# Kernel optimization log

Measured on AMD Instinct MI355X. Metric: run time of the kernel, lower is better.

The kernel has to match this reference:

```python
import jax, jax.numpy as jnp
import numpy as np

DIM = 384
WS = 7
NH = 12
N = WS ** 3          # 343 tokens per window
BW = 256             # number of windows (batch*num_windows)
HD = DIM // NH       # head dim = 32


def _rel_pos_index(ws: int) -> np.ndarray:
    coords = np.stack(np.meshgrid(np.arange(ws), np.arange(ws), np.arange(ws), indexing='ij'))
    coords = coords.reshape(3, -1)                       # [3, N]
    rel = coords[:, :, None] - coords[:, None, :]        # [3, N, N]
    rel = rel.transpose(1, 2, 0)                         # [N, N, 3]
    rel = rel + (ws - 1)
    idx = rel[..., 0] * (2 * ws - 1) ** 2 + rel[..., 1] * (2 * ws - 1) + rel[..., 2]
    return idx.astype(np.int32)                          # [N, N]


def setup_inputs() -> dict:
    key = jax.random.key(0)
    ks = jax.random.split(key, 6)
    x = jax.random.normal(ks[0], (BW, N, DIM), dtype=jnp.float32)
    qkv_w = jax.random.normal(ks[1], (DIM, 3 * DIM), dtype=jnp.float32) * (DIM ** -0.5)
    qkv_b = jax.random.normal(ks[2], (3 * DIM,), dtype=jnp.float32) * 0.02
    proj_w = jax.random.normal(ks[3], (DIM, DIM), dtype=jnp.float32) * (DIM ** -0.5)
    proj_b = jax.random.normal(ks[4], (DIM,), dtype=jnp.float32) * 0.02
    bias_table = jax.random.normal(ks[5], ((2 * WS - 1) ** 3, NH), dtype=jnp.float32) * 0.02
    rel_pos_index = jnp.asarray(_rel_pos_index(WS))
    return {"x": x, "qkv_w": qkv_w, "qkv_b": qkv_b, "proj_w": proj_w,
            "proj_b": proj_b, "bias_table": bias_table, "rel_pos_index": rel_pos_index}


def reference(x, qkv_w, qkv_b, proj_w, proj_b, bias_table, rel_pos_index):
    B_, n, C = x.shape
    scale = (C // NH) ** -0.5
    qkv = (x @ qkv_w + qkv_b).reshape(B_, n, 3, NH, C // NH)
    q, k, v = qkv[:, :, 0], qkv[:, :, 1], qkv[:, :, 2]   # [B_, n, H, d]
    # scores: [B_, H, n, n]
    attn = jnp.einsum('bihd,bjhd->bhij', q, k) * scale
    rel_bias = bias_table[rel_pos_index]                  # [n, n, H]
    attn = attn + rel_bias.transpose(2, 0, 1)[None]
    attn = jax.nn.softmax(attn, axis=-1)
    out = jnp.einsum('bhij,bjhd->bihd', attn, v).reshape(B_, n, C)
    return out @ proj_w + proj_b
```

## Files before the change

kernel.cpp:

```cpp
#include <hip/hip_runtime.h>


#define M_TOT 87808
#define NTOK  343
#define NPAD  352
#define DIMC  384
#define NHEAD 12
#define QKVN  1152
#define BWIN  256
#define BSLAB (NTOK * NPAD)

typedef __bf16 bf16x8 __attribute__((ext_vector_type(8)));
typedef __bf16 bf16x4 __attribute__((ext_vector_type(4)));
typedef float f32x4 __attribute__((ext_vector_type(4)));

__device__ __forceinline__ unsigned short bf16rne(float f) {
  unsigned int u = __float_as_uint(f);
  u += 0x7fffu + ((u >> 16) & 1u);
  return (unsigned short)(u >> 16);
}

__device__ __forceinline__ unsigned int packbf(float lo, float hi) {
  return (unsigned int)bf16rne(lo) | ((unsigned int)bf16rne(hi) << 16);
}

__device__ __forceinline__ bf16x4 pack_bf16x4(float a, float b, float c, float d) {
  unsigned ua = __float_as_uint(a) + 0x8000u;
  unsigned ub = __float_as_uint(b) + 0x8000u;
  unsigned uc = __float_as_uint(c) + 0x8000u;
  unsigned ud = __float_as_uint(d) + 0x8000u;
  unsigned lo = __builtin_amdgcn_perm(ub, ua, 0x07060302u);
  unsigned hi = __builtin_amdgcn_perm(ud, uc, 0x07060302u);
  union { unsigned u[2]; bf16x4 v; } x;
  x.u[0] = lo; x.u[1] = hi;
  return x.v;
}


__global__ void cvt_x_kernel(const float* __restrict__ x, unsigned short* __restrict__ xb, int n8) {
  int i = blockIdx.x * 256 + threadIdx.x;
  if (i >= n8) return;
  const float4* xv = (const float4*)x + (size_t)i * 2;
  float4 a = xv[0], b = xv[1];
  uint4 o;
  o.x = packbf(a.x, a.y); o.y = packbf(a.z, a.w);
  o.z = packbf(b.x, b.y); o.w = packbf(b.z, b.w);
  ((uint4*)xb)[i] = o;
}

__global__ void prep_w_kernel(const float* __restrict__ qkv_w, const float* __restrict__ proj_w,
                              unsigned short* __restrict__ wqkvT, unsigned short* __restrict__ wprojT) {
  int tid = blockIdx.x * 256 + threadIdx.x;
  if (tid < QKVN * DIMC) {
    int n = tid / DIMC, k = tid - n * DIMC;
    wqkvT[tid] = bf16rne(qkv_w[(size_t)k * QKVN + n]);
  }
  if (tid < DIMC * DIMC) {
    int n = tid / DIMC, k = tid - n * DIMC;
    wprojT[tid] = bf16rne(proj_w[(size_t)k * DIMC + n]);
  }
}

__global__ void prep_bias_kernel(const float* __restrict__ bias_table, const int* __restrict__ rel_idx,
                                 float* __restrict__ biasmat) {
  int tid = blockIdx.x * 256 + threadIdx.x;
  if (tid >= NTOK * NPAD) return;
  int i = tid / NPAD, j = tid - i * NPAD;
  const float LOG2E = 1.44269504088896340f;
  if (j < NTOK) {
    int idx = rel_idx[i * NTOK + j];
    #pragma unroll
    for (int h = 0; h < NHEAD; h++)
      biasmat[(size_t)h * BSLAB + tid] = bias_table[idx * NHEAD + h] * LOG2E;
  } else {
    #pragma unroll
    for (int h = 0; h < NHEAD; h++)
      biasmat[(size_t)h * BSLAB + tid] = -1e30f;
  }
}


typedef const __attribute__((address_space(1))) unsigned int* gas_t;
typedef __attribute__((address_space(3))) unsigned int* las_t;

__device__ __forceinline__ void load16_lds(const void* g, void* l) {
  __builtin_amdgcn_global_load_lds((gas_t)g, (las_t)l, 16, 0, 0);
}

template<int OUT_MODE>
__global__ __launch_bounds__(256, 3) void gemm_bt_kernel(
    const unsigned short* __restrict__ A, const unsigned short* __restrict__ Bt,
    const float* __restrict__ bias, void* __restrict__ outp,
    int M, int Nn, int K)
{
  __shared__ __attribute__((aligned(16))) unsigned short Atile[128 * 64];
  __shared__ __attribute__((aligned(16))) unsigned short Btile[128 * 64];
  const int t = threadIdx.x;
  const int lane = t & 63, w = t >> 6;
  const int q = lane >> 4, l15 = lane & 15;
  const int m0 = blockIdx.y * 128, n0 = blockIdx.x * 128;
  const int wm = w >> 1, wn = w & 1;

  f32x4 acc[4][4] = {};

  for (int kk = 0; kk < K; kk += 64) {
    #pragma unroll
    for (int i = 0; i < 4; i++) {
      int chunk = i * 256 + t;
      int r = chunk >> 3, cl = chunk & 7;
      int cg = cl ^ (r & 7);
      load16_lds(A + (size_t)(m0 + r) * K + kk + cg * 8, Atile + chunk * 8);
      load16_lds(Bt + (size_t)(n0 + r) * K + kk + cg * 8, Btile + chunk * 8);
    }
    __syncthreads();
    const bf16x8* As = (const bf16x8*)Atile;
    const bf16x8* Bs = (const bf16x8*)Btile;
    #pragma unroll
    for (int kq = 0; kq < 2; kq++) {
      bf16x8 af[4], bfr[4];
      #pragma unroll
      for (int mt = 0; mt < 4; mt++) {
        int m = wm * 64 + mt * 16 + l15;
        af[mt] = As[m * 8 + ((kq * 4 + q) ^ (m & 7))];
      }
      #pragma unroll
      for (int nt = 0; nt < 4; nt++) {
        int nr = wn * 64 + nt * 16 + l15;
        bfr[nt] = Bs[nr * 8 + ((kq * 4 + q) ^ (nr & 7))];
      }
      #pragma unroll
      for (int mt = 0; mt < 4; mt++)
        #pragma unroll
        for (int nt = 0; nt < 4; nt++)
          acc[mt][nt] = __builtin_amdgcn_mfma_f32_16x16x32_bf16(af[mt], bfr[nt], acc[mt][nt], 0, 0, 0);
    }
    __syncthreads();
  }

  #pragma unroll
  for (int nt = 0; nt < 4; nt++) {
    int nn = n0 + wn * 64 + nt * 16;
    float bv = bias[nn + l15];
    #pragma unroll
    for (int mt = 0; mt < 4; mt++) {
      int mb = m0 + wm * 64 + mt * 16 + q * 4;
      #pragma unroll
      for (int r = 0; r < 4; r++) {
        float v = acc[mt][nt][r] + bv;
        if (OUT_MODE == 0) {
          ((float*)outp)[(size_t)(mb + r) * Nn + nn + l15] = v;
        } else {
          int which = nn / DIMC;
          int hh = (nn - which * DIMC) >> 5;
          int d0 = nn & 16;
          size_t off = ((size_t)(which * NHEAD + hh) * M_TOT + (mb + r)) * 32 + d0 + l15;
          ((unsigned short*)outp)[off] = bf16rne(v);
        }
      }
    }
  }
}


#define VST 360

__global__ __launch_bounds__(512, 6) void attn_kernel(
    const unsigned short* __restrict__ qhead,
    const float* __restrict__ biasmat,
    unsigned short* __restrict__ attnout)
{
  __shared__ __attribute__((aligned(16))) unsigned short Klds[22 * 512];
  __shared__ __attribute__((aligned(16))) unsigned short Vt[32 * VST];
  const int bx = blockIdx.x;
  const int h = bx >> 8, b = bx & 255;
  const int t = threadIdx.x;
  const int lane = t & 63, w = t >> 6;
  const int q = lane >> 4, l15 = lane & 15;

  const unsigned short* Qslab = qhead + ((size_t)(0 * NHEAD + h) * M_TOT + (size_t)b * NTOK) * 32;
  const unsigned short* Kslab = qhead + ((size_t)(1 * NHEAD + h) * M_TOT + (size_t)b * NTOK) * 32;
  const unsigned short* Vslab = qhead + ((size_t)(2 * NHEAD + h) * M_TOT + (size_t)b * NTOK) * 32;

  for (int jt = w; jt < 22; jt += 8)
    load16_lds(Kslab + (size_t)(jt * 16 + l15) * 32 + q * 8, Klds + jt * 512 + lane * 8);

  for (int j = t; j < NTOK; j += 512) {
    #pragma unroll
    for (int c = 0; c < 4; c++) {
      uint4 vd = *(const uint4*)(Vslab + (size_t)j * 32 + c * 8);
      const unsigned short* vs = (const unsigned short*)&vd;
      #pragma unroll
      for (int u = 0; u < 8; u++)
        Vt[(c * 8 + u) * VST + j] = vs[u];
    }
  }
  for (int idx = t; idx < 32 * 16; idx += 512)
    Vt[(idx >> 4) * VST + NTOK + (idx & 15)] = 0;
  __syncthreads();

  const float* bh_bias = biasmat + (size_t)h * BSLAB;
  const float CS = 0.17677669529663689f * 1.44269504088896340f;

  for (int pr = w; pr < 11; pr += 8) {
    int i0 = pr * 32;
    int iqA = i0 + l15;      iqA = iqA > (NTOK - 1) ? (NTOK - 1) : iqA;
    int iqB = i0 + 16 + l15; iqB = iqB > (NTOK - 1) ? (NTOK - 1) : iqB;
    bf16x8 bqA = *(const bf16x8*)(Qslab + (size_t)iqA * 32 + q * 8);
    bf16x8 bqB = *(const bf16x8*)(Qslab + (size_t)iqB * 32 + q * 8);
    const float* browA = bh_bias + (size_t)iqA * NPAD + 4 * q;
    const float* browB = bh_bias + (size_t)iqB * NPAD + 4 * q;

    f32x4 oA0 = {0.f,0.f,0.f,0.f}, oA1 = {0.f,0.f,0.f,0.f};
    f32x4 oB0 = {0.f,0.f,0.f,0.f}, oB1 = {0.f,0.f,0.f,0.f};
    float denA = 0.f, denB = 0.f;

    #pragma unroll 2
    for (int jt = 0; jt < 22; jt++) {
      bf16x8 ak = *(const bf16x8*)(Klds + jt * 512 + lane * 8);
      f32x4 z = {0.f,0.f,0.f,0.f};
      f32x4 sA = __builtin_amdgcn_mfma_f32_16x16x32_bf16(ak, bqA, z, 0, 0, 0);
      f32x4 sB = __builtin_amdgcn_mfma_f32_16x16x32_bf16(ak, bqB, z, 0, 0, 0);
      f32x4 bA = *(const f32x4*)(browA + jt * 16);
      f32x4 bB = *(const f32x4*)(browB + jt * 16);
      float pA0 = __builtin_amdgcn_exp2f(fmaf(sA[0], CS, bA[0]));
      float pA1 = __builtin_amdgcn_exp2f(fmaf(sA[1], CS, bA[1]));
      float pA2 = __builtin_amdgcn_exp2f(fmaf(sA[2], CS, bA[2]));
      float pA3 = __builtin_amdgcn_exp2f(fmaf(sA[3], CS, bA[3]));
      float pB0 = __builtin_amdgcn_exp2f(fmaf(sB[0], CS, bB[0]));
      float pB1 = __builtin_amdgcn_exp2f(fmaf(sB[1], CS, bB[1]));
      float pB2 = __builtin_amdgcn_exp2f(fmaf(sB[2], CS, bB[2]));
      float pB3 = __builtin_amdgcn_exp2f(fmaf(sB[3], CS, bB[3]));
      denA += (pA0 + pA1) + (pA2 + pA3);
      denB += (pB0 + pB1) + (pB2 + pB3);
      bf16x4 pfA = pack_bf16x4(pA0, pA1, pA2, pA3);
      bf16x4 pfB = pack_bf16x4(pB0, pB1, pB2, pB3);
      bf16x4 vf0 = *(const bf16x4*)(Vt + l15 * VST + jt * 16 + 4 * q);
      bf16x4 vf1 = *(const bf16x4*)(Vt + (16 + l15) * VST + jt * 16 + 4 * q);
      oA0 = __builtin_amdgcn_mfma_f32_16x16x16bf16_1k(pfA, vf0, oA0, 0, 0, 0);
      oA1 = __builtin_amdgcn_mfma_f32_16x16x16bf16_1k(pfA, vf1, oA1, 0, 0, 0);
      oB0 = __builtin_amdgcn_mfma_f32_16x16x16bf16_1k(pfB, vf0, oB0, 0, 0, 0);
      oB1 = __builtin_amdgcn_mfma_f32_16x16x16bf16_1k(pfB, vf1, oB1, 0, 0, 0);
    }

    denA += __shfl_xor(denA, 16); denA += __shfl_xor(denA, 32);
    denB += __shfl_xor(denB, 16); denB += __shfl_xor(denB, 32);

    #pragma unroll
    for (int r = 0; r < 4; r++) {
      int rr = 4 * q + r;
      float dA = __shfl(denA, rr);
      float dB = __shfl(denB, rr);
      int iA = i0 + rr, iB = i0 + 16 + rr;
      if (iA < NTOK) {
        float inv = __builtin_amdgcn_rcpf(dA);
        size_t orow = ((size_t)b * NTOK + iA) * DIMC + h * 32;
        attnout[orow + l15]      = bf16rne(oA0[r] * inv);
        attnout[orow + 16 + l15] = bf16rne(oA1[r] * inv);
      }
      if (iB < NTOK) {
        float inv = __builtin_amdgcn_rcpf(dB);
        size_t orow = ((size_t)b * NTOK + iB) * DIMC + h * 32;
        attnout[orow + l15]      = bf16rne(oB0[r] * inv);
        attnout[orow + 16 + l15] = bf16rne(oB1[r] * inv);
      }
    }
  }
}


extern "C" void kernel_launch(void* const* d_in, const int* in_sizes, int n_in,
                              void* d_out, int out_size, void* d_ws, size_t ws_size,
                              hipStream_t stream) {
  const float* x          = (const float*)d_in[0];
  const float* qkv_w      = (const float*)d_in[1];
  const float* qkv_b      = (const float*)d_in[2];
  const float* proj_w     = (const float*)d_in[3];
  const float* proj_b     = (const float*)d_in[4];
  const float* bias_table = (const float*)d_in[5];
  const int*   rel_idx    = (const int*)d_in[6];

  char* p = (char*)d_ws;
  unsigned short* xb      = (unsigned short*)p; p += (size_t)M_TOT * DIMC * 2;
  unsigned short* wqkvT   = (unsigned short*)p; p += (size_t)QKVN * DIMC * 2;
  unsigned short* wprojT  = (unsigned short*)p; p += (size_t)DIMC * DIMC * 2;
  float*          biasmat = (float*)p;          p += (size_t)NHEAD * BSLAB * 4;
  unsigned short* qhead   = (unsigned short*)p; p += (size_t)3 * NHEAD * M_TOT * 32 * 2;
  unsigned short* attnout = (unsigned short*)p; p += (size_t)M_TOT * DIMC * 2;

  cvt_x_kernel<<<(M_TOT * DIMC / 8 + 255) / 256, 256, 0, stream>>>(x, xb, M_TOT * DIMC / 8);
  prep_w_kernel<<<(QKVN * DIMC + 255) / 256, 256, 0, stream>>>(qkv_w, proj_w, wqkvT, wprojT);
  prep_bias_kernel<<<(NTOK * NPAD + 255) / 256, 256, 0, stream>>>(bias_table, rel_idx, biasmat);
  gemm_bt_kernel<1><<<dim3(QKVN / 128, M_TOT / 128), 256, 0, stream>>>(
      xb, wqkvT, qkv_b, (void*)qhead, M_TOT, QKVN, DIMC);
  attn_kernel<<<BWIN * NHEAD, 512, 0, stream>>>(qhead, biasmat, attnout);
  gemm_bt_kernel<0><<<dim3(DIMC / 128, M_TOT / 128), 256, 0, stream>>>(
      attnout, wprojT, proj_b, d_out, M_TOT, DIMC, DIMC);
}
```

Before: 631.1 us.

## Store relative-position bias as tiled bf16 and prefetch it in attention loop

New measurement: 894.4 us. 41.7% more time.

```diff
diff --git a/kernel.cpp b/kernel.cpp
--- a/kernel.cpp
+++ b/kernel.cpp
@@ -3,16 +3,16 @@
 
 #define M_TOT 87808
 #define NTOK  343
-#define NPAD  352
 #define DIMC  384
 #define NHEAD 12
 #define QKVN  1152
 #define BWIN  256
-#define BSLAB (NTOK * NPAD)
+#define TSLAB (22 * 22 * 256)
 
 typedef __bf16 bf16x8 __attribute__((ext_vector_type(8)));
 typedef __bf16 bf16x4 __attribute__((ext_vector_type(4)));
 typedef float f32x4 __attribute__((ext_vector_type(4)));
+typedef unsigned short u16x4 __attribute__((ext_vector_type(4)));
 
 __device__ __forceinline__ unsigned short bf16rne(float f) {
   unsigned int u = __float_as_uint(f);
@@ -36,6 +36,10 @@
   return x.v;
 }
 
+__device__ __forceinline__ float bf16tof(unsigned short s) {
+  return __uint_as_float(((unsigned int)s) << 16);
+}
+
 
 __global__ void cvt_x_kernel(const float* __restrict__ x, unsigned short* __restrict__ xb, int n8) {
   int i = blockIdx.x * 256 + threadIdx.x;
@@ -61,22 +65,32 @@
   }
 }
 
-__global__ void prep_bias_kernel(const float* __restrict__ bias_table, const int* __restrict__ rel_idx,
-                                 float* __restrict__ biasmat) {
+__global__ void prep_biasT_kernel(const float* __restrict__ bias_table, const int* __restrict__ rel_idx,
+                                  unsigned short* __restrict__ biasT) {
   int tid = blockIdx.x * 256 + threadIdx.x;
-  if (tid >= NTOK * NPAD) return;
-  int i = tid / NPAD, j = tid - i * NPAD;
+  if (tid >= NHEAD * 22 * 22 * 64) return;
+  int l15 = tid & 15;
+  int q   = (tid >> 4) & 3;
+  int rest = tid >> 6;
+  int jt  = rest % 22;
+  int it  = (rest / 22) % 22;
+  int h   = rest / (22 * 22);
+  int i = it * 16 + l15; if (i > NTOK - 1) i = NTOK - 1;
   const float LOG2E = 1.44269504088896340f;
-  if (j < NTOK) {
-    int idx = rel_idx[i * NTOK + j];
-    #pragma unroll
-    for (int h = 0; h < NHEAD; h++)
-      biasmat[(size_t)h * BSLAB + tid] = bias_table[idx * NHEAD + h] * LOG2E;
-  } else {
-    #pragma unroll
-    for (int h = 0; h < NHEAD; h++)
-      biasmat[(size_t)h * BSLAB + tid] = -1e30f;
-  }
+  u16x4 out;
+  #pragma unroll
+  for (int r = 0; r < 4; r++) {
+    int j = jt * 16 + 4 * q + r;
+    float v;
+    if (j < NTOK) {
+      int idx = rel_idx[i * NTOK + j];
+      v = bias_table[idx * NHEAD + h] * LOG2E;
+    } else {
+      v = -1e30f;
+    }
+    out[r] = bf16rne(v);
+  }
+  *(u16x4*)(biasT + (size_t)tid * 4) = out;
 }
 
 
@@ -164,15 +178,19 @@
 
 #define VST 360
 
-__global__ __launch_bounds__(512, 6) void attn_kernel(
+__global__ __launch_bounds__(512, 4) void attn_kernel(
     const unsigned short* __restrict__ qhead,
-    const float* __restrict__ biasmat,
+    const unsigned short* __restrict__ biasT,
     unsigned short* __restrict__ attnout)
 {
   __shared__ __attribute__((aligned(16))) unsigned short Klds[22 * 512];
   __shared__ __attribute__((aligned(16))) unsigned short Vt[32 * VST];
   const int bx = blockIdx.x;
-  const int h = bx >> 8, b = bx & 255;
+  const int g = bx & 7, s = bx >> 3;
+  int h, b;
+  if (s < 256) { h = g; b = s; }
+  else { int j = g * 128 + (s - 256); h = 8 + (j >> 8); b = j & 255; }
+
   const int t = threadIdx.x;
   const int lane = t & 63, w = t >> 6;
   const int q = lane >> 4, l15 = lane & 15;
@@ -198,7 +216,6 @@
     Vt[(idx >> 4) * VST + NTOK + (idx & 15)] = 0;
   __syncthreads();
 
-  const float* bh_bias = biasmat + (size_t)h * BSLAB;
   const float CS = 0.17677669529663689f * 1.44269504088896340f;
 
   for (int pr = w; pr < 11; pr += 8) {
@@ -207,29 +224,41 @@
     int iqB = i0 + 16 + l15; iqB = iqB > (NTOK - 1) ? (NTOK - 1) : iqB;
     bf16x8 bqA = *(const bf16x8*)(Qslab + (size_t)iqA * 32 + q * 8);
     bf16x8 bqB = *(const bf16x8*)(Qslab + (size_t)iqB * 32 + q * 8);
-    const float* browA = bh_bias + (size_t)iqA * NPAD + 4 * q;
-    const float* browB = bh_bias + (size_t)iqB * NPAD + 4 * q;
+
+    const unsigned short* bApt = biasT + ((size_t)(h * 22 + pr * 2) * 22) * 256 + q * 64 + l15 * 4;
+    const unsigned short* bBpt = bApt + 22 * 256;
+
+    u16x4 bufA[4], bufB[4];
+    #pragma unroll
+    for (int pf = 0; pf < 4; pf++) {
+      bufA[pf] = *(const u16x4*)(bApt + pf * 256);
+      bufB[pf] = *(const u16x4*)(bBpt + pf * 256);
+    }
 
     f32x4 oA0 = {0.f,0.f,0.f,0.f}, oA1 = {0.f,0.f,0.f,0.f};
     f32x4 oB0 = {0.f,0.f,0.f,0.f}, oB1 = {0.f,0.f,0.f,0.f};
     float denA = 0.f, denB = 0.f;
 
-    #pragma unroll 2
+    #pragma unroll
     for (int jt = 0; jt < 22; jt++) {
       bf16x8 ak = *(const bf16x8*)(Klds + jt * 512 + lane * 8);
       f32x4 z = {0.f,0.f,0.f,0.f};
       f32x4 sA = __builtin_amdgcn_mfma_f32_16x16x32_bf16(ak, bqA, z, 0, 0, 0);
       f32x4 sB = __builtin_amdgcn_mfma_f32_16x16x32_bf16(ak, bqB, z, 0, 0, 0);
-      f32x4 bA = *(const f32x4*)(browA + jt * 16);
-      f32x4 bB = *(const f32x4*)(browB + jt * 16);
-      float pA0 = __builtin_amdgcn_exp2f(fmaf(sA[0], CS, bA[0]));
-      float pA1 = __builtin_amdgcn_exp2f(fmaf(sA[1], CS, bA[1]));
-      float pA2 = __builtin_amdgcn_exp2f(fmaf(sA[2], CS, bA[2]));
-      float pA3 = __builtin_amdgcn_exp2f(fmaf(sA[3], CS, bA[3]));
-      float pB0 = __builtin_amdgcn_exp2f(fmaf(sB[0], CS, bB[0]));
-      float pB1 = __builtin_amdgcn_exp2f(fmaf(sB[1], CS, bB[1]));
-      float pB2 = __builtin_amdgcn_exp2f(fmaf(sB[2], CS, bB[2]));
-      float pB3 = __builtin_amdgcn_exp2f(fmaf(sB[3], CS, bB[3]));
+      u16x4 cbA = bufA[jt & 3];
+      u16x4 cbB = bufB[jt & 3];
+      if (jt + 4 < 22) {
+        bufA[jt & 3] = *(const u16x4*)(bApt + (jt + 4) * 256);
+        bufB[jt & 3] = *(const u16x4*)(bBpt + (jt + 4) * 256);
+      }
+      float pA0 = __builtin_amdgcn_exp2f(fmaf(sA[0], CS, bf16tof(cbA[0])));
+      float pA1 = __builtin_amdgcn_exp2f(fmaf(sA[1], CS, bf16tof(cbA[1])));
+      float pA2 = __builtin_amdgcn_exp2f(fmaf(sA[2], CS, bf16tof(cbA[2])));
+      float pA3 = __builtin_amdgcn_exp2f(fmaf(sA[3], CS, bf16tof(cbA[3])));
+      float pB0 = __builtin_amdgcn_exp2f(fmaf(sB[0], CS, bf16tof(cbB[0])));
+      float pB1 = __builtin_amdgcn_exp2f(fmaf(sB[1], CS, bf16tof(cbB[1])));
+      float pB2 = __builtin_amdgcn_exp2f(fmaf(sB[2], CS, bf16tof(cbB[2])));
+      float pB3 = __builtin_amdgcn_exp2f(fmaf(sB[3], CS, bf16tof(cbB[3])));
       denA += (pA0 + pA1) + (pA2 + pA3);
       denB += (pB0 + pB1) + (pB2 + pB3);
       bf16x4 pfA = pack_bf16x4(pA0, pA1, pA2, pA3);
@@ -283,16 +312,16 @@
   unsigned short* xb      = (unsigned short*)p; p += (size_t)M_TOT * DIMC * 2;
   unsigned short* wqkvT   = (unsigned short*)p; p += (size_t)QKVN * DIMC * 2;
   unsigned short* wprojT  = (unsigned short*)p; p += (size_t)DIMC * DIMC * 2;
-  float*          biasmat = (float*)p;          p += (size_t)NHEAD * BSLAB * 4;
+  unsigned short* biasT   = (unsigned short*)p; p += (size_t)NHEAD * TSLAB * 2;
   unsigned short* qhead   = (unsigned short*)p; p += (size_t)3 * NHEAD * M_TOT * 32 * 2;
   unsigned short* attnout = (unsigned short*)p; p += (size_t)M_TOT * DIMC * 2;
 
   cvt_x_kernel<<<(M_TOT * DIMC / 8 + 255) / 256, 256, 0, stream>>>(x, xb, M_TOT * DIMC / 8);
   prep_w_kernel<<<(QKVN * DIMC + 255) / 256, 256, 0, stream>>>(qkv_w, proj_w, wqkvT, wprojT);
-  prep_bias_kernel<<<(NTOK * NPAD + 255) / 256, 256, 0, stream>>>(bias_table, rel_idx, biasmat);
+  prep_biasT_kernel<<<(NHEAD * 22 * 22 * 64 + 255) / 256, 256, 0, stream>>>(bias_table, rel_idx, biasT);
   gemm_bt_kernel<1><<<dim3(QKVN / 128, M_TOT / 128), 256, 0, stream>>>(
       xb, wqkvT, qkv_b, (void*)qhead, M_TOT, QKVN, DIMC);
-  attn_kernel<<<BWIN * NHEAD, 512, 0, stream>>>(qhead, biasmat, attnout);
+  attn_kernel<<<BWIN * NHEAD, 512, 0, stream>>>(qhead, biasT, attnout);
   gemm_bt_kernel<0><<<dim3(DIMC / 128, M_TOT / 128), 256, 0, stream>>>(
       attnout, wprojT, proj_b, d_out, M_TOT, DIMC, DIMC);
 }
```
